# Kernel tuning notes

Hardware: AMD Instinct MI355X
Metric: run time of the kernel (lower is better)

Reference implementation:

```python
import jax, jax.numpy as jnp
import numpy as np

TAGSET = 50
START_TAG = 48
END_TAG = 49
SEQ_LEN = 512
BATCH = 64
HIDDEN = 512


def setup_inputs() -> dict:
    key = jax.random.key(0)
    k1, k2, k3, k4 = jax.random.split(key, 4)
    feats = jax.random.normal(k1, (SEQ_LEN, BATCH, HIDDEN), dtype=jnp.float32)
    W = jax.random.normal(k2, (TAGSET * TAGSET, HIDDEN), dtype=jnp.float32) * (1.0 / np.sqrt(HIDDEN))
    b = jax.random.normal(k3, (TAGSET * TAGSET,), dtype=jnp.float32) * 0.01
    target = jax.random.randint(k4, (SEQ_LEN, BATCH, 1), 0, TAGSET * TAGSET, dtype=jnp.int64)
    mask = jnp.ones((SEQ_LEN, BATCH), dtype=bool)
    return {"feats": feats, "W": W, "b": b, "target": target, "mask": mask}


def reference(feats, W, b, target, mask):
    S, B, H = feats.shape
    T = TAGSET
    # hidden2tag: Linear(H -> T*T), then view (S, B, T_from, T_to)
    scores = jnp.einsum('sbh,kh->sbk', feats, W) + b  # (S, B, T*T)
    scores4 = scores.reshape(S, B, T, T)

    # gold-path energy: gather flattened (from,to) index per position, mask, sum
    tg_energy = jnp.take_along_axis(scores, target, axis=2)[..., 0]  # (S, B)
    tg_sum = jnp.sum(jnp.where(mask, tg_energy, jnp.zeros((), scores.dtype)))

    # forward algorithm (log-sum-exp semiring scan over time)
    partition0 = scores4[0, :, START_TAG, :]  # (B, T)

    def step(partition, xs):
        cur, m = xs  # cur: (B, T_from, T_to), m: (B,)
        new = jax.nn.logsumexp(cur + partition[:, :, None], axis=1)  # (B, T)
        partition = jnp.where(m[:, None], new, partition)
        return partition, None

    partition, _ = jax.lax.scan(step, partition0, (scores4[1:], mask[1:]))
    loss = (jnp.sum(partition[:, END_TAG]) - tg_sum) / B
    return loss
```

## Files before the change

kernel.cpp:

```cpp
#include <hip/hip_runtime.h>
#include <math.h>


#define KK    2500
#define KPAD  2560
#define NROW  32768
#define MTS   72
#define MTS2  80
#define LN2   0.69314718055994530942f
#define LOG2E 1.44269504088896340736f

typedef __attribute__((ext_vector_type(8))) short short8;
typedef __attribute__((ext_vector_type(8))) unsigned short ushort8;
typedef __attribute__((ext_vector_type(4))) float f32x4;

__device__ __forceinline__ unsigned short f2bf(float f){
  unsigned int u = __builtin_bit_cast(unsigned int, f);
  u += 0x7fffu + ((u >> 16) & 1u);
  return (unsigned short)(u >> 16);
}
__device__ __forceinline__ float bf2f(unsigned short h){
  return __builtin_bit_cast(float, ((unsigned int)h) << 16);
}
__device__ __forceinline__ void gload_lds16(const unsigned short* g, unsigned short* l){
  __builtin_amdgcn_global_load_lds((const __attribute__((address_space(1))) void*)g,
                                   (__attribute__((address_space(3))) void*)l,
                                   16, 0, 0);
}

__global__ __launch_bounds__(256) void init_kernel(const float* __restrict__ bias_in,
                                                   float* __restrict__ bias_pad,
                                                   float* __restrict__ out){
  int i = blockIdx.x * 256 + threadIdx.x;
  if (i < KPAD) bias_pad[i] = (i < KK) ? bias_in[i] : 0.0f;
  if (i == 0) out[0] = 0.0f;
}

__global__ __launch_bounds__(256) void cvt_kernel(const float* __restrict__ s,
                                                  unsigned short* __restrict__ d,
                                                  int n_src, int n_tot){
  int i = (blockIdx.x * 256 + threadIdx.x) << 3;
  if (i >= n_tot) return;
  ushort8 o = {0,0,0,0,0,0,0,0};
  if (i < n_src){
    f32x4 a = *(const f32x4*)(s + i);
    f32x4 b = *(const f32x4*)(s + i + 4);
    o[0]=f2bf(a[0]); o[1]=f2bf(a[1]); o[2]=f2bf(a[2]); o[3]=f2bf(a[3]);
    o[4]=f2bf(b[0]); o[5]=f2bf(b[1]); o[6]=f2bf(b[2]); o[7]=f2bf(b[3]);
  }
  *(ushort8*)(d + i) = o;
}

__global__ __launch_bounds__(256) void gemm_exp_kernel(
    const unsigned short* __restrict__ A,
    const unsigned short* __restrict__ Bw,
    const float* __restrict__ bias,
    unsigned short* __restrict__ E)
{
  __shared__ alignas(16) unsigned short As[128 * 32];
  __shared__ alignas(16) unsigned short Bs[128 * 32];
  const int t = threadIdx.x;
  const int lane = t & 63, w = t >> 6;
  const int Rbase = blockIdx.y * 128;
  const int Cbase = blockIdx.x * 128;
  const int m0 = (w >> 1) * 64, n0 = (w & 1) * 64;
  const int fr = lane & 15;
  const int fk = (lane >> 4) * 8;
  const int lrow = lane >> 2;
  const int lcol = (lane & 3) * 8;
  const unsigned short* Ag0 = A + (size_t)(Rbase + w * 32 + lrow) * 512 + lcol;
  const unsigned short* Ag1 = Ag0 + 16 * 512;
  const unsigned short* Bg0 = Bw + (size_t)(Cbase + w * 32 + lrow) * 512 + lcol;
  const unsigned short* Bg1 = Bg0 + 16 * 512;
  unsigned short* Al0 = &As[(w * 32) * 32];
  unsigned short* Al1 = &As[(w * 32 + 16) * 32];
  unsigned short* Bl0 = &Bs[(w * 32) * 32];
  unsigned short* Bl1 = &Bs[(w * 32 + 16) * 32];

  f32x4 acc[4][4];
  const f32x4 vz = {0.f, 0.f, 0.f, 0.f};
  #pragma unroll
  for (int i = 0; i < 4; i++)
    #pragma unroll
    for (int j = 0; j < 4; j++) acc[i][j] = vz;

  for (int kt = 0; kt < 16; kt++){
    const int k0 = kt * 32;
    gload_lds16(Ag0 + k0, Al0);
    gload_lds16(Ag1 + k0, Al1);
    gload_lds16(Bg0 + k0, Bl0);
    gload_lds16(Bg1 + k0, Bl1);
    __syncthreads();
    short8 af[4], bf[4];
    #pragma unroll
    for (int mf = 0; mf < 4; mf++) af[mf] = *(const short8*)&As[(m0 + mf * 16 + fr) * 32 + fk];
    #pragma unroll
    for (int nf = 0; nf < 4; nf++) bf[nf] = *(const short8*)&Bs[(n0 + nf * 16 + fr) * 32 + fk];
    #pragma unroll
    for (int mf = 0; mf < 4; mf++)
      #pragma unroll
      for (int nf = 0; nf < 4; nf++)
        acc[mf][nf] = __builtin_amdgcn_mfma_f32_16x16x32_bf16(af[mf], bf[nf], acc[mf][nf], 0, 0, 0);
    __syncthreads();
  }
  #pragma unroll
  for (int nf = 0; nf < 4; nf++){
    const int C = Cbase + n0 + nf * 16 + fr;
    const float bv = bias[C];
    #pragma unroll
    for (int mf = 0; mf < 4; mf++){
      const int Rb = Rbase + m0 + mf * 16 + (lane >> 4) * 4;
      #pragma unroll
      for (int r = 0; r < 4; r++){
        float sc = acc[mf][nf][r] + bv;
        float e = exp2f(sc * LOG2E - 9.0f);
        E[(size_t)(Rb + r) * KPAD + C] = f2bf(e);
      }
    }
  }
}

__global__ __launch_bounds__(256) void gather_kernel(const unsigned short* __restrict__ E,
                                                     const int* __restrict__ target,
                                                     float* __restrict__ out){
  const int t = threadIdx.x;
  const int idx = blockIdx.x * 256 + t;
  float v = 0.0f;
  if (idx < NROW){
    int kt = target[idx];
    v = logf(bf2f(E[(size_t)idx * KPAD + kt])) + 9.0f * LN2;
  }
  for (int off = 32; off; off >>= 1) v += __shfl_xor(v, off);
  __shared__ float r4[4];
  if ((t & 63) == 0) r4[t >> 6] = v;
  __syncthreads();
  if (t == 0) atomicAdd(out, -(r4[0] + r4[1] + r4[2] + r4[3]) * (1.0f / 64.0f));
}

__global__ __launch_bounds__(256) void chunk_prod_kernel(const unsigned short* __restrict__ E,
                                                         unsigned short* __restrict__ Pc,
                                                         float* __restrict__ lsc){
  const int c = blockIdx.x, b = blockIdx.y;
  const int s0 = 1 + c * 8;
  const int L = (s0 + 8 <= 512) ? 8 : (512 - s0);
  __shared__ alignas(16) unsigned short Pl[64 * MTS];
  __shared__ alignas(16) unsigned short Mt[64 * MTS];
  __shared__ float red[4];
  const int t = threadIdx.x;
  const int lane = t & 63, w = t >> 6;
  const int m0 = (w >> 1) * 32, n0 = (w & 1) * 32;
  const int fr = lane & 15, fk = (lane >> 4) * 8;

  for (int i = t; i < 64 * MTS; i += 256){ Pl[i] = 0; Mt[i] = 0; }
  __syncthreads();
  {
    const unsigned short* rowp = E + (size_t)(s0 * 64 + b) * KPAD;
    ushort8 x0 = *(const ushort8*)(rowp + t * 8);
    #pragma unroll
    for (int u = 0; u < 8; u++){ int k = t * 8 + u; Pl[(k / 50) * MTS + (k % 50)] = x0[u]; }
    if (t < 57){
      ushort8 x1 = *(const ushort8*)(rowp + (t + 256) * 8);
      #pragma unroll
      for (int u = 0; u < 8; u++){ int k = (t + 256) * 8 + u; if (k < KK) Pl[(k / 50) * MTS + (k % 50)] = x1[u]; }
    }
  }
  ushort8 rg0 = {0,0,0,0,0,0,0,0}, rg1 = {0,0,0,0,0,0,0,0};
  {
    const unsigned short* rowp = E + (size_t)((s0 + 1) * 64 + b) * KPAD;
    rg0 = *(const ushort8*)(rowp + t * 8);
    if (t < 57) rg1 = *(const ushort8*)(rowp + (t + 256) * 8);
  }
  f32x4 acc[2][2];
  const f32x4 vz = {0.f, 0.f, 0.f, 0.f};
  for (int step = 1; step < L; step++){
    {
      #pragma unroll
      for (int u = 0; u < 8; u++){ int k = t * 8 + u; Mt[(k % 50) * MTS + (k / 50)] = rg0[u]; }
      if (t < 57){
        #pragma unroll
        for (int u = 0; u < 8; u++){ int k = (t + 256) * 8 + u; if (k < KK) Mt[(k % 50) * MTS + (k / 50)] = rg1[u]; }
      }
    }
    if (step > 1){
      #pragma unroll
      for (int mf = 0; mf < 2; mf++)
        #pragma unroll
        for (int nf = 0; nf < 2; nf++)
          #pragma unroll
          for (int r = 0; r < 4; r++){
            int mm = m0 + mf * 16 + (lane >> 4) * 4 + r;
            int nn = n0 + nf * 16 + fr;
            Pl[mm * MTS + nn] = f2bf(acc[mf][nf][r]);
          }
    }
    __syncthreads();
    if (step + 1 < L){
      const unsigned short* rowp = E + (size_t)((s0 + step + 1) * 64 + b) * KPAD;
      rg0 = *(const ushort8*)(rowp + t * 8);
      if (t < 57) rg1 = *(const ushort8*)(rowp + (t + 256) * 8);
    }
    acc[0][0] = vz; acc[0][1] = vz; acc[1][0] = vz; acc[1][1] = vz;
    #pragma unroll
    for (int ks = 0; ks < 2; ks++){
      const int k0 = ks * 32 + fk;
      short8 a0 = *(const short8*)&Pl[(m0 + fr) * MTS + k0];
      short8 a1 = *(const short8*)&Pl[(m0 + 16 + fr) * MTS + k0];
      short8 b0 = *(const short8*)&Mt[(n0 + fr) * MTS + k0];
      short8 b1 = *(const short8*)&Mt[(n0 + 16 + fr) * MTS + k0];
      acc[0][0] = __builtin_amdgcn_mfma_f32_16x16x32_bf16(a0, b0, acc[0][0], 0, 0, 0);
      acc[0][1] = __builtin_amdgcn_mfma_f32_16x16x32_bf16(a0, b1, acc[0][1], 0, 0, 0);
      acc[1][0] = __builtin_amdgcn_mfma_f32_16x16x32_bf16(a1, b0, acc[1][0], 0, 0, 0);
      acc[1][1] = __builtin_amdgcn_mfma_f32_16x16x32_bf16(a1, b1, acc[1][1], 0, 0, 0);
    }
    __syncthreads();
  }
  float mx = 0.0f;
  #pragma unroll
  for (int mf = 0; mf < 2; mf++)
    #pragma unroll
    for (int nf = 0; nf < 2; nf++)
      #pragma unroll
      for (int r = 0; r < 4; r++) mx = fmaxf(mx, acc[mf][nf][r]);
  for (int off = 32; off; off >>= 1) mx = fmaxf(mx, __shfl_xor(mx, off));
  if (lane == 0) red[w] = mx;
  __syncthreads();
  float gmax = fmaxf(fmaxf(red[0], red[1]), fmaxf(red[2], red[3]));
  float inv = 1.0f / gmax;
  unsigned short* outp = Pc + (size_t)(b * 64 + c) * 4096;
  #pragma unroll
  for (int mf = 0; mf < 2; mf++)
    #pragma unroll
    for (int nf = 0; nf < 2; nf++)
      #pragma unroll
      for (int r = 0; r < 4; r++){
        int mm = m0 + mf * 16 + (lane >> 4) * 4 + r;
        int nn = n0 + nf * 16 + fr;
        outp[mm * 64 + nn] = f2bf(acc[mf][nf][r] * inv);
      }
  if (t == 0) lsc[b * 64 + c] = logf(gmax) + (float)L * 9.0f * LN2;
}

__global__ __launch_bounds__(256) void quad_prod_kernel(const unsigned short* __restrict__ In,
                                                        const float* __restrict__ lsin,
                                                        unsigned short* __restrict__ Out,
                                                        float* __restrict__ lsout,
                                                        int ncin){
  const int jo = blockIdx.x, b = blockIdx.y, ncout = gridDim.x;
  const size_t base = ((size_t)b * ncin + jo * 4) * 4096;
  __shared__ alignas(16) unsigned short Pl[64 * MTS2];
  __shared__ alignas(16) unsigned short Mt[64 * MTS2];
  __shared__ float red[4];
  const int t = threadIdx.x;
  const int lane = t & 63, w = t >> 6;
  const int m0 = (w >> 1) * 32, n0 = (w & 1) * 32;
  const int fr = lane & 15, fk = (lane >> 4) * 8;
  for (int i = t; i < 64 * MTS2; i += 256){ Pl[i] = 0; Mt[i] = 0; }
  __syncthreads();
  {
    const ushort8* src = (const ushort8*)(In + base);
    ushort8 x0 = src[t], x1 = src[t + 256];
    *(ushort8*)&Pl[(t >> 3) * MTS2 + (t & 7) * 8] = x0;
    *(ushort8*)&Pl[((t + 256) >> 3) * MTS2 + (t & 7) * 8] = x1;
  }
  f32x4 acc[2][2];
  const f32x4 vz = {0.f, 0.f, 0.f, 0.f};
  for (int f = 1; f < 4; f++){
    const ushort8* src = (const ushort8*)(In + base + (size_t)f * 4096);
    ushort8 x0 = src[t], x1 = src[t + 256];
    {
      int k0c = t >> 3, nb = (t & 7) * 8;
      #pragma unroll
      for (int i = 0; i < 8; i++) Mt[(nb + i) * MTS2 + k0c] = x0[i];
      int k1c = (t + 256) >> 3;
      #pragma unroll
      for (int i = 0; i < 8; i++) Mt[(nb + i) * MTS2 + k1c] = x1[i];
    }
    if (f > 1){
      #pragma unroll
      for (int mf = 0; mf < 2; mf++)
        #pragma unroll
        for (int nf = 0; nf < 2; nf++)
          #pragma unroll
          for (int r = 0; r < 4; r++){
            int mm = m0 + mf * 16 + (lane >> 4) * 4 + r;
            int nn = n0 + nf * 16 + fr;
            Pl[mm * MTS2 + nn] = f2bf(acc[mf][nf][r]);
          }
    }
    __syncthreads();
    acc[0][0] = vz; acc[0][1] = vz; acc[1][0] = vz; acc[1][1] = vz;
    #pragma unroll
    for (int ks = 0; ks < 2; ks++){
      const int k0 = ks * 32 + fk;
      short8 a0 = *(const short8*)&Pl[(m0 + fr) * MTS2 + k0];
      short8 a1 = *(const short8*)&Pl[(m0 + 16 + fr) * MTS2 + k0];
      short8 b0 = *(const short8*)&Mt[(n0 + fr) * MTS2 + k0];
      short8 b1 = *(const short8*)&Mt[(n0 + 16 + fr) * MTS2 + k0];
      acc[0][0] = __builtin_amdgcn_mfma_f32_16x16x32_bf16(a0, b0, acc[0][0], 0, 0, 0);
      acc[0][1] = __builtin_amdgcn_mfma_f32_16x16x32_bf16(a0, b1, acc[0][1], 0, 0, 0);
      acc[1][0] = __builtin_amdgcn_mfma_f32_16x16x32_bf16(a1, b0, acc[1][0], 0, 0, 0);
      acc[1][1] = __builtin_amdgcn_mfma_f32_16x16x32_bf16(a1, b1, acc[1][1], 0, 0, 0);
    }
    __syncthreads();
  }
  float mx = 0.0f;
  #pragma unroll
  for (int mf = 0; mf < 2; mf++)
    #pragma unroll
    for (int nf = 0; nf < 2; nf++)
      #pragma unroll
      for (int r = 0; r < 4; r++) mx = fmaxf(mx, acc[mf][nf][r]);
  for (int off = 32; off; off >>= 1) mx = fmaxf(mx, __shfl_xor(mx, off));
  if (lane == 0) red[w] = mx;
  __syncthreads();
  float gmax = fmaxf(fmaxf(red[0], red[1]), fmaxf(red[2], red[3]));
  float inv = 1.0f / gmax;
  unsigned short* outp = Out + ((size_t)b * ncout + jo) * 4096;
  #pragma unroll
  for (int mf = 0; mf < 2; mf++)
    #pragma unroll
    for (int nf = 0; nf < 2; nf++)
      #pragma unroll
      for (int r = 0; r < 4; r++){
        int mm = m0 + mf * 16 + (lane >> 4) * 4 + r;
        int nn = n0 + nf * 16 + fr;
        outp[mm * 64 + nn] = f2bf(acc[mf][nf][r] * inv);
      }
  if (t == 0){
    const float* lp = lsin + (size_t)b * ncin + jo * 4;
    lsout[(size_t)b * ncout + jo] = lp[0] + lp[1] + lp[2] + lp[3] + logf(gmax);
  }
}

__global__ __launch_bounds__(64) void finish_kernel(const unsigned short* __restrict__ E,
                                                    const unsigned short* __restrict__ Pt,
                                                    const float* __restrict__ ls,
                                                    float* __restrict__ out){
  const int b = blockIdx.x, t = threadIdx.x;
  float v = 0.0f;
  if (t < 50){
    float p0 = bf2f(E[(size_t)b * KPAD + 48 * 50 + t]);
    float pe = bf2f(Pt[(size_t)b * 4096 + t * 64 + 49]);
    v = p0 * pe;
  }
  for (int off = 32; off; off >>= 1) v += __shfl_xor(v, off);
  if (t == 0) atomicAdd(out, (logf(v) + 9.0f * LN2 + ls[b]) * (1.0f / 64.0f));
}

extern "C" void kernel_launch(void* const* d_in, const int* in_sizes, int n_in,
                              void* d_out, int out_size, void* d_ws, size_t ws_size,
                              hipStream_t stream){
  const float* feats  = (const float*)d_in[0];
  const float* W      = (const float*)d_in[1];
  const float* bias   = (const float*)d_in[2];
  const int*   target = (const int*)d_in[3];
  float* out = (float*)d_out;
  char* ws = (char*)d_ws;
  unsigned short* Abf  = (unsigned short*)(ws + 0);
  unsigned short* Wbf  = (unsigned short*)(ws + 33554432);
  float*          bpad = (float*)(ws + 36175872);
  unsigned short* E    = (unsigned short*)(ws + 36186112);
  unsigned short* Pc   = (unsigned short*)(ws + 203958272);
  float*          lsc  = (float*)(ws + 237512704);
  unsigned short* T1   = (unsigned short*)(ws + 0);
  unsigned short* T2   = (unsigned short*)(ws + 8388608);
  unsigned short* T3   = (unsigned short*)(ws + 10485760);
  float*          ls1  = (float*)(ws + 11010048);
  float*          ls2  = (float*)(ws + 11014144);
  float*          ls3  = (float*)(ws + 11015168);

  init_kernel<<<10, 256, 0, stream>>>(bias, bpad, out);
  cvt_kernel<<<8192, 256, 0, stream>>>(feats, Abf, 16777216, 16777216);
  cvt_kernel<<<640, 256, 0, stream>>>(W, Wbf, 1280000, 1310720);
  gemm_exp_kernel<<<dim3(20, 256), 256, 0, stream>>>(Abf, Wbf, bpad, E);
  gather_kernel<<<128, 256, 0, stream>>>(E, target, out);
  chunk_prod_kernel<<<dim3(64, 64), 256, 0, stream>>>(E, Pc, lsc);
  quad_prod_kernel<<<dim3(16, 64), 256, 0, stream>>>(Pc, lsc, T1, ls1, 64);
  quad_prod_kernel<<<dim3(4, 64), 256, 0, stream>>>(T1, ls1, T2, ls2, 16);
  quad_prod_kernel<<<dim3(1, 64), 256, 0, stream>>>(T2, ls2, T3, ls3, 4);
  finish_kernel<<<64, 64, 0, stream>>>(E, T3, ls3, out);
}
```

Measured before the change: 318.8 us.

## Fuse prep kernels, gold-score gather into GEMM epilogue, and use 8-way product tree

Merges the bias-init and two bf16 conversion kernels into one launch. The gold-path gather moves into the GEMM epilogue, which compares columns to targets and sums the exact fp32 score instead of re-reading bf16 exp values. The epilogue now stages E through LDS so global stores are coalesced 16-byte writes. The three 4-way product reduction levels plus the finish kernel become two 8-way levels, the last folding in the finish step. This cuts launches and improves store efficiency, at the cost of extra LDS, syncs and a target load per row in the GEMM epilogue.

```diff
diff --git a/kernel.cpp b/kernel.cpp
--- a/kernel.cpp
+++ b/kernel.cpp
@@ -28,37 +28,51 @@
                                    16, 0, 0);
 }
 
-__global__ __launch_bounds__(256) void init_kernel(const float* __restrict__ bias_in,
+__global__ __launch_bounds__(256) void prep_kernel(const float* __restrict__ feats,
+                                                   const float* __restrict__ W,
+                                                   const float* __restrict__ bias_in,
+                                                   unsigned short* __restrict__ Abf,
+                                                   unsigned short* __restrict__ Wbf,
                                                    float* __restrict__ bias_pad,
                                                    float* __restrict__ out){
-  int i = blockIdx.x * 256 + threadIdx.x;
-  if (i < KPAD) bias_pad[i] = (i < KK) ? bias_in[i] : 0.0f;
-  if (i == 0) out[0] = 0.0f;
-}
-
-__global__ __launch_bounds__(256) void cvt_kernel(const float* __restrict__ s,
-                                                  unsigned short* __restrict__ d,
-                                                  int n_src, int n_tot){
-  int i = (blockIdx.x * 256 + threadIdx.x) << 3;
-  if (i >= n_tot) return;
-  ushort8 o = {0,0,0,0,0,0,0,0};
-  if (i < n_src){
-    f32x4 a = *(const f32x4*)(s + i);
-    f32x4 b = *(const f32x4*)(s + i + 4);
+  const int bid = blockIdx.x, t = threadIdx.x;
+  if (bid < 8192){
+    const int i = (bid * 256 + t) << 3;
+    f32x4 a = *(const f32x4*)(feats + i);
+    f32x4 b = *(const f32x4*)(feats + i + 4);
+    ushort8 o;
     o[0]=f2bf(a[0]); o[1]=f2bf(a[1]); o[2]=f2bf(a[2]); o[3]=f2bf(a[3]);
     o[4]=f2bf(b[0]); o[5]=f2bf(b[1]); o[6]=f2bf(b[2]); o[7]=f2bf(b[3]);
-  }
-  *(ushort8*)(d + i) = o;
+    *(ushort8*)(Abf + i) = o;
+  } else if (bid < 8832){
+    const int i = ((bid - 8192) * 256 + t) << 3;
+    ushort8 o = {0,0,0,0,0,0,0,0};
+    if (i < 1280000){
+      f32x4 a = *(const f32x4*)(W + i);
+      f32x4 b = *(const f32x4*)(W + i + 4);
+      o[0]=f2bf(a[0]); o[1]=f2bf(a[1]); o[2]=f2bf(a[2]); o[3]=f2bf(a[3]);
+      o[4]=f2bf(b[0]); o[5]=f2bf(b[1]); o[6]=f2bf(b[2]); o[7]=f2bf(b[3]);
+    }
+    *(ushort8*)(Wbf + i) = o;
+  } else {
+    const int i = (bid - 8832) * 256 + t;
+    if (i < KPAD) bias_pad[i] = (i < KK) ? bias_in[i] : 0.0f;
+    if (i == 0) out[0] = 0.0f;
+  }
 }
 
 __global__ __launch_bounds__(256) void gemm_exp_kernel(
     const unsigned short* __restrict__ A,
     const unsigned short* __restrict__ Bw,
     const float* __restrict__ bias,
-    unsigned short* __restrict__ E)
+    const int* __restrict__ target,
+    unsigned short* __restrict__ E,
+    float* __restrict__ out)
 {
   __shared__ alignas(16) unsigned short As[128 * 32];
   __shared__ alignas(16) unsigned short Bs[128 * 32];
+  __shared__ alignas(16) unsigned short Ep[64 * 128];
+  __shared__ float r4[4];
   const int t = threadIdx.x;
   const int lane = t & 63, w = t >> 6;
   const int Rbase = blockIdx.y * 128;
@@ -103,36 +117,41 @@
         acc[mf][nf] = __builtin_amdgcn_mfma_f32_16x16x32_bf16(af[mf], bf[nf], acc[mf][nf], 0, 0, 0);
     __syncthreads();
   }
-  #pragma unroll
-  for (int nf = 0; nf < 4; nf++){
-    const int C = Cbase + n0 + nf * 16 + fr;
-    const float bv = bias[C];
-    #pragma unroll
-    for (int mf = 0; mf < 4; mf++){
-      const int Rb = Rbase + m0 + mf * 16 + (lane >> 4) * 4;
+  float tsum = 0.0f;
+  float bv[4];
+  #pragma unroll
+  for (int nf = 0; nf < 4; nf++) bv[nf] = bias[Cbase + n0 + nf * 16 + fr];
+  #pragma unroll
+  for (int h = 0; h < 2; h++){
+    #pragma unroll
+    for (int mh = 0; mh < 2; mh++){
+      const int mf = 2 * h + mh;
       #pragma unroll
       for (int r = 0; r < 4; r++){
-        float sc = acc[mf][nf][r] + bv;
-        float e = exp2f(sc * LOG2E - 9.0f);
-        E[(size_t)(Rb + r) * KPAD + C] = f2bf(e);
+        const int gm = Rbase + m0 + mf * 16 + (lane >> 4) * 4 + r;
+        const int tg = target[gm];
+        const int lr = (w >> 1) * 32 + mh * 16 + (lane >> 4) * 4 + r;
+        #pragma unroll
+        for (int nf = 0; nf < 4; nf++){
+          const float sc = acc[mf][nf][r] + bv[nf];
+          const int gc = Cbase + n0 + nf * 16 + fr;
+          if (gc == tg) tsum += sc;
+          Ep[lr * 128 + (w & 1) * 64 + nf * 16 + fr] = f2bf(exp2f(sc * LOG2E - 9.0f));
+        }
       }
     }
-  }
-}
-
-__global__ __launch_bounds__(256) void gather_kernel(const unsigned short* __restrict__ E,
-                                                     const int* __restrict__ target,
-                                                     float* __restrict__ out){
-  const int t = threadIdx.x;
-  const int idx = blockIdx.x * 256 + t;
-  float v = 0.0f;
-  if (idx < NROW){
-    int kt = target[idx];
-    v = logf(bf2f(E[(size_t)idx * KPAD + kt])) + 9.0f * LN2;
-  }
-  for (int off = 32; off; off >>= 1) v += __shfl_xor(v, off);
-  __shared__ float r4[4];
-  if ((t & 63) == 0) r4[t >> 6] = v;
+    __syncthreads();
+    #pragma unroll
+    for (int q = 0; q < 4; q++){
+      const int c = t + q * 256;
+      const int lr = c >> 4, coff = (c & 15) * 8;
+      const int gm = Rbase + h * 32 + (lr & 31) + (lr >> 5) * 64;
+      *(ushort8*)&E[(size_t)gm * KPAD + Cbase + coff] = *(const ushort8*)&Ep[lr * 128 + coff];
+    }
+    __syncthreads();
+  }
+  for (int off = 32; off; off >>= 1) tsum += __shfl_xor(tsum, off);
+  if (lane == 0) r4[w] = tsum;
   __syncthreads();
   if (t == 0) atomicAdd(out, -(r4[0] + r4[1] + r4[2] + r4[3]) * (1.0f / 64.0f));
 }
@@ -240,13 +259,15 @@
   if (t == 0) lsc[b * 64 + c] = logf(gmax) + (float)L * 9.0f * LN2;
 }
 
-__global__ __launch_bounds__(256) void quad_prod_kernel(const unsigned short* __restrict__ In,
-                                                        const float* __restrict__ lsin,
-                                                        unsigned short* __restrict__ Out,
-                                                        float* __restrict__ lsout,
-                                                        int ncin){
+__global__ __launch_bounds__(256) void oct_prod_kernel(const unsigned short* __restrict__ In,
+                                                       const float* __restrict__ lsin,
+                                                       unsigned short* __restrict__ Out,
+                                                       float* __restrict__ lsout,
+                                                       int ncin, int fan,
+                                                       const unsigned short* __restrict__ E,
+                                                       float* __restrict__ out, int finish){
   const int jo = blockIdx.x, b = blockIdx.y, ncout = gridDim.x;
-  const size_t base = ((size_t)b * ncin + jo * 4) * 4096;
+  const size_t base = ((size_t)b * ncin + jo * fan) * 4096;
   __shared__ alignas(16) unsigned short Pl[64 * MTS2];
   __shared__ alignas(16) unsigned short Mt[64 * MTS2];
   __shared__ float red[4];
@@ -264,7 +285,7 @@
   }
   f32x4 acc[2][2];
   const f32x4 vz = {0.f, 0.f, 0.f, 0.f};
-  for (int f = 1; f < 4; f++){
+  for (int f = 1; f < fan; f++){
     const ushort8* src = (const ushort8*)(In + base + (size_t)f * 4096);
     ushort8 x0 = src[t], x1 = src[t + 256];
     {
@@ -315,36 +336,48 @@
   __syncthreads();
   float gmax = fmaxf(fmaxf(red[0], red[1]), fmaxf(red[2], red[3]));
   float inv = 1.0f / gmax;
-  unsigned short* outp = Out + ((size_t)b * ncout + jo) * 4096;
-  #pragma unroll
-  for (int mf = 0; mf < 2; mf++)
-    #pragma unroll
-    for (int nf = 0; nf < 2; nf++)
-      #pragma unroll
-      for (int r = 0; r < 4; r++){
-        int mm = m0 + mf * 16 + (lane >> 4) * 4 + r;
-        int nn = n0 + nf * 16 + fr;
-        outp[mm * 64 + nn] = f2bf(acc[mf][nf][r] * inv);
+  if (!finish){
+    unsigned short* outp = Out + ((size_t)b * ncout + jo) * 4096;
+    #pragma unroll
+    for (int mf = 0; mf < 2; mf++)
+      #pragma unroll
+      for (int nf = 0; nf < 2; nf++)
+        #pragma unroll
+        for (int r = 0; r < 4; r++){
+          int mm = m0 + mf * 16 + (lane >> 4) * 4 + r;
+          int nn = n0 + nf * 16 + fr;
+          outp[mm * 64 + nn] = f2bf(acc[mf][nf][r] * inv);
+        }
+    if (t == 0){
+      const float* lp = lsin + (size_t)b * ncin + jo * fan;
+      float s = 0.0f;
+      for (int i = 0; i < fan; i++) s += lp[i];
+      lsout[(size_t)b * ncout + jo] = s + logf(gmax);
+    }
+  } else {
+    #pragma unroll
+    for (int mf = 0; mf < 2; mf++)
+      #pragma unroll
+      for (int nf = 0; nf < 2; nf++)
+        #pragma unroll
+        for (int r = 0; r < 4; r++){
+          int mm = m0 + mf * 16 + (lane >> 4) * 4 + r;
+          int nn = n0 + nf * 16 + fr;
+          Pl[mm * MTS2 + nn] = f2bf(acc[mf][nf][r] * inv);
+        }
+    __syncthreads();
+    if (t < 64){
+      float p0 = (t < 50) ? bf2f(E[(size_t)b * KPAD + 48 * 50 + t]) : 0.0f;
+      float v = p0 * bf2f(Pl[t * MTS2 + 49]);
+      for (int off = 32; off; off >>= 1) v += __shfl_xor(v, off);
+      if (t == 0){
+        const float* lp = lsin + (size_t)b * ncin + jo * fan;
+        float s = 0.0f;
+        for (int i = 0; i < fan; i++) s += lp[i];
+        atomicAdd(out, (logf(v) + 9.0f * LN2 + s + logf(gmax)) * (1.0f / 64.0f));
       }
-  if (t == 0){
-    const float* lp = lsin + (size_t)b * ncin + jo * 4;
-    lsout[(size_t)b * ncout + jo] = lp[0] + lp[1] + lp[2] + lp[3] + logf(gmax);
-  }
-}
-
-__global__ __launch_bounds__(64) void finish_kernel(const unsigned short* __restrict__ E,
-                                                    const unsigned short* __restrict__ Pt,
-                                                    const float* __restrict__ ls,
-                                                    float* __restrict__ out){
-  const int b = blockIdx.x, t = threadIdx.x;
-  float v = 0.0f;
-  if (t < 50){
-    float p0 = bf2f(E[(size_t)b * KPAD + 48 * 50 + t]);
-    float pe = bf2f(Pt[(size_t)b * 4096 + t * 64 + 49]);
-    v = p0 * pe;
-  }
-  for (int off = 32; off; off >>= 1) v += __shfl_xor(v, off);
-  if (t == 0) atomicAdd(out, (logf(v) + 9.0f * LN2 + ls[b]) * (1.0f / 64.0f));
+    }
+  }
 }
 
 extern "C" void kernel_launch(void* const* d_in, const int* in_sizes, int n_in,
@@ -363,20 +396,11 @@
   unsigned short* Pc   = (unsigned short*)(ws + 203958272);
   float*          lsc  = (float*)(ws + 237512704);
   unsigned short* T1   = (unsigned short*)(ws + 0);
-  unsigned short* T2   = (unsigned short*)(ws + 8388608);
-  unsigned short* T3   = (unsigned short*)(ws + 10485760);
-  float*          ls1  = (float*)(ws + 11010048);
-  float*          ls2  = (float*)(ws + 11014144);
-  float*          ls3  = (float*)(ws + 11015168);
-
-  init_kernel<<<10, 256, 0, stream>>>(bias, bpad, out);
-  cvt_kernel<<<8192, 256, 0, stream>>>(feats, Abf, 16777216, 16777216);
-  cvt_kernel<<<640, 256, 0, stream>>>(W, Wbf, 1280000, 1310720);
-  gemm_exp_kernel<<<dim3(20, 256), 256, 0, stream>>>(Abf, Wbf, bpad, E);
-  gather_kernel<<<128, 256, 0, stream>>>(E, target, out);
+  float*          ls1  = (float*)(ws + 4194304);
+
+  prep_kernel<<<8842, 256, 0, stream>>>(feats, W, bias, Abf, Wbf, bpad, out);
+  gemm_exp_kernel<<<dim3(20, 256), 256, 0, stream>>>(Abf, Wbf, bpad, target, E, out);
   chunk_prod_kernel<<<dim3(64, 64), 256, 0, stream>>>(E, Pc, lsc);
-  quad_prod_kernel<<<dim3(16, 64), 256, 0, stream>>>(Pc, lsc, T1, ls1, 64);
-  quad_prod_kernel<<<dim3(4, 64), 256, 0, stream>>>(T1, ls1, T2, ls2, 16);
-  quad_prod_kernel<<<dim3(1, 64), 256, 0, stream>>>(T2, ls2, T3, ls3, 4);
-  finish_kernel<<<64, 64, 0, stream>>>(E, T3, ls3, out);
-}
+  oct_prod_kernel<<<dim3(8, 64), 256, 0, stream>>>(Pc, lsc, T1, ls1, 64, 8, E, out, 0);
+  oct_prod_kernel<<<dim3(1, 64), 256, 0, stream>>>(T1, ls1, T1, ls1, 8, 8, E, out, 1);
+}
```

After: 324.9 us. About the same (+1.9%).
